# Performance work log

Measured on AMD Instinct MI355X. Metric: run time of the kernel, lower is better.

The kernel has to match this reference:

```python
import jax, jax.numpy as jnp
import numpy as np

NW, S, D, H, F = 4096, 64, 128, 8, 256
DH = D // H
EPS = 1e-5


def setup_inputs() -> dict:
    key = jax.random.key(0)
    ks = jax.random.split(key, 16)
    feat = jax.random.normal(ks[0], (NW, S, D), jnp.float32)
    pos = 0.1 * jax.random.normal(ks[1], (NW, S, D), jnp.float32)
    # each window has between S//2 and S valid voxels; True = padded key
    valid = jax.random.randint(ks[2], (NW, 1), S // 2, S + 1)
    mask = jnp.arange(S)[None, :] >= valid  # [NW, S] bool
    s = 1.0 / np.sqrt(D)
    u = lambda k, sh, sc: jax.random.uniform(k, sh, jnp.float32, -sc, sc)
    return {
        'feat': feat, 'pos': pos, 'mask': mask,
        'Wq': u(ks[3], (D, D), s), 'bq': jnp.zeros((D,), jnp.float32),
        'Wk': u(ks[4], (D, D), s), 'bk': jnp.zeros((D,), jnp.float32),
        'Wv': u(ks[5], (D, D), s), 'bv': jnp.zeros((D,), jnp.float32),
        'Wo': u(ks[6], (D, D), s), 'bo': jnp.zeros((D,), jnp.float32),
        'W1': u(ks[7], (D, F), s), 'b1': jnp.zeros((F,), jnp.float32),
        'W2': u(ks[8], (F, D), 1.0 / np.sqrt(F)), 'b2': jnp.zeros((D,), jnp.float32),
        'g1': jnp.ones((D,), jnp.float32), 'be1': jnp.zeros((D,), jnp.float32),
        'g2': jnp.ones((D,), jnp.float32), 'be2': jnp.zeros((D,), jnp.float32),
    }


def _layernorm(x, g, b):
    mu = jnp.mean(x, -1, keepdims=True)
    var = jnp.mean(jnp.square(x - mu), -1, keepdims=True)
    return (x - mu) * jax.lax.rsqrt(var + EPS) * g + b


def reference(feat, pos, mask, Wq, bq, Wk, bk, Wv, bv, Wo, bo,
              W1, b1, W2, b2, g1, be1, g2, be2):
    # windowed MHA: q = k = feat + pos, v = feat  (all windows batched)
    qk_in = feat + pos
    q = (qk_in @ Wq + bq).reshape(NW, S, H, DH)
    k = (qk_in @ Wk + bk).reshape(NW, S, H, DH)
    v = (feat @ Wv + bv).reshape(NW, S, H, DH)
    scores = jnp.einsum('wqhd,wkhd->whqk', q, k) / np.sqrt(DH)
    scores = jnp.where(mask[:, None, None, :], -1e9, scores)
    attn = jax.nn.softmax(scores, axis=-1)
    ctx = jnp.einsum('whqk,wkhd->wqhd', attn, v).reshape(NW, S, D)
    src2 = ctx @ Wo + bo
    # residual + LN + FFN + residual + LN (dropout = identity at eval)
    src = _layernorm(feat + src2, g1, be1)
    ffn = jax.nn.relu(src @ W1 + b1) @ W2 + b2
    return _layernorm(src + ffn, g2, be2)
```

## Files before the change

kernel.cpp:

```cpp
#include <hip/hip_runtime.h>

typedef __attribute__((ext_vector_type(8))) short bf16x8;
typedef __attribute__((ext_vector_type(4))) float f32x4;
typedef unsigned short u16;
typedef unsigned int u32;

#define MFMA16(a, b, c) __builtin_amdgcn_mfma_f32_16x16x32_bf16((a), (b), (c), 0, 0, 0)
#define CFENCE() asm volatile("" ::: "memory")


__device__ __forceinline__ u16 f2bf(float f) {
    union { float f; u32 u; } c; c.f = f;
    u32 r = c.u + 0x7fffu + ((c.u >> 16) & 1u);
    return (u16)(r >> 16);
}

__device__ __forceinline__ bf16x8 pack8(f32x4 a, f32x4 b) {
    union { u32 w[4]; bf16x8 v; } r;
    asm("v_cvt_pk_bf16_f32 %0, %1, %2" : "=v"(r.w[0]) : "v"(a[0]), "v"(a[1]));
    asm("v_cvt_pk_bf16_f32 %0, %1, %2" : "=v"(r.w[1]) : "v"(a[2]), "v"(a[3]));
    asm("v_cvt_pk_bf16_f32 %0, %1, %2" : "=v"(r.w[2]) : "v"(b[0]), "v"(b[1]));
    asm("v_cvt_pk_bf16_f32 %0, %1, %2" : "=v"(r.w[3]) : "v"(b[2]), "v"(b[3]));
    return r.v;
}

__device__ __forceinline__ void stage_h(const float* __restrict__ W, int ld,
                                        int n0, int k0, u16* __restrict__ sW,
                                        int t) {
#pragma unroll
    for (int i = 0; i < 4; ++i) {
        int e = i * 512 + t;
        int n = e & 63, kq = e >> 6;
        const float* src = W + (size_t)(k0 + kq * 4) * ld + n0 + n;
        float a = src[0], b = src[ld], c = src[2 * ld], d = src[3 * ld];
        u32 lo, hi;
        asm("v_cvt_pk_bf16_f32 %0, %1, %2" : "=v"(lo) : "v"(a), "v"(b));
        asm("v_cvt_pk_bf16_f32 %0, %1, %2" : "=v"(hi) : "v"(c), "v"(d));
        uint2 pk; pk.x = lo; pk.y = hi;
        *(uint2*)(sW + n * 136 + kq * 4) = pk;
    }
}

__device__ __forceinline__ void gemm_h(const bf16x8 aF[4], const u16* __restrict__ sW,
                                       int lr, int lk, f32x4 acc[4]) {
#pragma unroll
    for (int ks = 0; ks < 4; ++ks)
#pragma unroll
        for (int nt = 0; nt < 4; ++nt) {
            bf16x8 b = *(const bf16x8*)(sW + (nt * 16 + lr) * 136 + ks * 32 + lk * 8);
            acc[nt] = MFMA16(aF[ks], b, acc[nt]);
        }
}

__device__ __forceinline__ void row_ln(const f32x4 v[8], float mu[4], float rs[4]) {
#pragma unroll
    for (int r = 0; r < 4; ++r) {
        float s = 0.f;
#pragma unroll
        for (int nt = 0; nt < 8; ++nt) s += v[nt][r];
        s += __shfl_xor(s, 1); s += __shfl_xor(s, 2);
        s += __shfl_xor(s, 4); s += __shfl_xor(s, 8);
        float m_ = s * 0.0078125f;
        float q = 0.f;
#pragma unroll
        for (int nt = 0; nt < 8; ++nt) { float d = v[nt][r] - m_; q += d * d; }
        q += __shfl_xor(q, 1); q += __shfl_xor(q, 2);
        q += __shfl_xor(q, 4); q += __shfl_xor(q, 8);
        mu[r] = m_;
        rs[r] = rsqrtf(q * 0.0078125f + 1e-5f);
    }
}

__global__ __launch_bounds__(512) void enc_main(
    const float* __restrict__ feat, const float* __restrict__ pos,
    const unsigned char* __restrict__ maskb,
    const float* __restrict__ Wq, const float* __restrict__ bq,
    const float* __restrict__ Wk, const float* __restrict__ bk,
    const float* __restrict__ Wv, const float* __restrict__ bv,
    const float* __restrict__ Wo, const float* __restrict__ bo,
    const float* __restrict__ W1, const float* __restrict__ b1,
    const float* __restrict__ W2, const float* __restrict__ b2,
    const float* __restrict__ g1, const float* __restrict__ be1,
    const float* __restrict__ g2, const float* __restrict__ be2,
    float* __restrict__ out) {
    __shared__ __align__(16) char smem[142336];

    const int tid  = threadIdx.x;
    const int lane = tid & 63;
    const int wid  = tid >> 6;
    const int ww   = wid >> 2;
    const int m0   = (wid & 3) * 16;
    const int lr   = lane & 15;
    const int lk   = lane >> 4;
    const int w    = blockIdx.x * 2 + ww;

    char* wb   = smem + ww * 62464;
    u16* sQ    = (u16*)wb;
    u16* sK    = (u16*)(wb + 17408);
    u16* sVt   = (u16*)(wb + 34816);
    u16* sAttn = (u16*)(wb + 53248);
    u16* sF1   = (u16*)(wb + 17408);
    u16* sW    = (u16*)(smem + 124928);

    const float* fw = feat + (size_t)w * 8192;
    const float* pw = pos  + (size_t)w * 8192;

    stage_h(Wq, 128, 0, 0, sW, tid);

    int vld;
    {
        unsigned char smp = maskb[lane * 64 + 63];
        int ones = __popcll(__ballot(smp != 0));
        int m = (ones > 32) ? (maskb[(size_t)w * 64 + lane] != 0)
                            : (((const int*)maskb)[(size_t)w * 64 + lane] != 0);
        vld = 64 - __popcll(__ballot(m));
    }

    bf16x8 aX[4], aFv[4];
#pragma unroll
    for (int ks = 0; ks < 4; ++ks) {
        const float* fp = fw + (m0 + lr) * 128 + ks * 32 + lk * 8;
        const float* pp = pw + (m0 + lr) * 128 + ks * 32 + lk * 8;
        f32x4 f0 = *(const f32x4*)fp;
        f32x4 f1 = *(const f32x4*)(fp + 4);
        f32x4 p0 = *(const f32x4*)pp;
        f32x4 p1 = *(const f32x4*)(pp + 4);
        aFv[ks] = pack8(f0, f1);
        aX[ks]  = pack8(f0 + p0, f1 + p1);
    }
    __syncthreads();

#pragma unroll
    for (int hf = 0; hf < 2; ++hf) {
        f32x4 acc[4] = {};
        gemm_h(aX, sW, lr, lk, acc);
#pragma unroll
        for (int nt = 0; nt < 4; ++nt) {
            int col = hf * 64 + nt * 16 + lr; float bb = bq[col];
#pragma unroll
            for (int r = 0; r < 4; ++r)
                sQ[(m0 + lk * 4 + r) * 136 + col] = f2bf(acc[nt][r] + bb);
        }
        __syncthreads();
        if (hf == 0) stage_h(Wq, 128, 64, 0, sW, tid);
        else         stage_h(Wk, 128, 0, 0, sW, tid);
        __syncthreads();
    }
#pragma unroll
    for (int hf = 0; hf < 2; ++hf) {
        f32x4 acc[4] = {};
        gemm_h(aX, sW, lr, lk, acc);
#pragma unroll
        for (int nt = 0; nt < 4; ++nt) {
            int col = hf * 64 + nt * 16 + lr; float bb = bk[col];
#pragma unroll
            for (int r = 0; r < 4; ++r)
                sK[(m0 + lk * 4 + r) * 136 + col] = f2bf(acc[nt][r] + bb);
        }
        __syncthreads();
        if (hf == 0) stage_h(Wk, 128, 64, 0, sW, tid);
        else         stage_h(Wv, 128, 0, 0, sW, tid);
        __syncthreads();
    }
#pragma unroll
    for (int hf = 0; hf < 2; ++hf) {
        f32x4 acc[4] = {};
        gemm_h(aFv, sW, lr, lk, acc);
#pragma unroll
        for (int nt = 0; nt < 4; ++nt) {
            int dcol = hf * 64 + nt * 16 + lr; float bb = bv[dcol];
            float e0 = acc[nt][0] + bb, e1 = acc[nt][1] + bb;
            float e2 = acc[nt][2] + bb, e3 = acc[nt][3] + bb;
            u32 lo, hi;
            asm("v_cvt_pk_bf16_f32 %0, %1, %2" : "=v"(lo) : "v"(e0), "v"(e1));
            asm("v_cvt_pk_bf16_f32 %0, %1, %2" : "=v"(hi) : "v"(e2), "v"(e3));
            uint2 pk; pk.x = lo; pk.y = hi;
            *(uint2*)(sVt + dcol * 72 + m0 + lk * 4) = pk;
        }
        __syncthreads();
        if (hf == 0) { stage_h(Wv, 128, 64, 0, sW, tid); __syncthreads(); }
    }

    stage_h(Wo, 128, 0, 0, sW, tid);
    const int dup = (lk & 1) * 8;
#pragma unroll 1
    for (int h = 0; h < 8; ++h) {
        bf16x8 aQ = *(const bf16x8*)(sQ + (m0 + lr) * 136 + h * 16 + dup);
        f32x4 sc[4];
#pragma unroll
        for (int nt = 0; nt < 4; ++nt) {
            bf16x8 bK = *(const bf16x8*)(sK + (nt * 16 + lr) * 136 + h * 16 + dup);
            f32x4 zz = {0.f, 0.f, 0.f, 0.f};
            sc[nt] = MFMA16(aQ, bK, zz);
        }
#pragma unroll
        for (int nt = 0; nt < 4; ++nt) {
            bool msk = (nt * 16 + lr) >= vld;
#pragma unroll
            for (int r = 0; r < 4; ++r) {
                float v0 = sc[nt][r] * 0.125f;
                sc[nt][r] = msk ? -1e9f : v0;
            }
        }
        float mx[4], sm[4];
#pragma unroll
        for (int r = 0; r < 4; ++r) {
            float m_ = fmaxf(fmaxf(sc[0][r], sc[1][r]), fmaxf(sc[2][r], sc[3][r]));
            m_ = fmaxf(m_, __shfl_xor(m_, 1));
            m_ = fmaxf(m_, __shfl_xor(m_, 2));
            m_ = fmaxf(m_, __shfl_xor(m_, 4));
            m_ = fmaxf(m_, __shfl_xor(m_, 8));
            mx[r] = m_; sm[r] = 0.f;
        }
#pragma unroll
        for (int nt = 0; nt < 4; ++nt)
#pragma unroll
            for (int r = 0; r < 4; ++r) {
                float e = __expf(sc[nt][r] - mx[r]);
                sc[nt][r] = e; sm[r] += e;
            }
#pragma unroll
        for (int r = 0; r < 4; ++r) {
            float s_ = sm[r];
            s_ += __shfl_xor(s_, 1); s_ += __shfl_xor(s_, 2);
            s_ += __shfl_xor(s_, 4); s_ += __shfl_xor(s_, 8);
            sm[r] = 1.f / s_;
        }
#pragma unroll
        for (int nt = 0; nt < 4; ++nt)
#pragma unroll
            for (int r = 0; r < 4; ++r)
                sAttn[(m0 + lk * 4 + r) * 72 + nt * 16 + lr] = f2bf(sc[nt][r] * sm[r]);
        CFENCE();
        f32x4 cc = {0.f, 0.f, 0.f, 0.f};
#pragma unroll
        for (int ks = 0; ks < 2; ++ks) {
            bf16x8 aP = *(const bf16x8*)(sAttn + (m0 + lr) * 72 + ks * 32 + lk * 8);
            bf16x8 bV = *(const bf16x8*)(sVt + (h * 16 + lr) * 72 + ks * 32 + lk * 8);
            cc = MFMA16(aP, bV, cc);
        }
#pragma unroll
        for (int r = 0; r < 4; ++r)
            sQ[(m0 + lk * 4 + r) * 136 + h * 16 + lr] = f2bf(cc[r]);
    }
    CFENCE();
    __syncthreads();

    bf16x8 aC[4];
#pragma unroll
    for (int ks = 0; ks < 4; ++ks)
        aC[ks] = *(const bf16x8*)(sQ + (m0 + lr) * 136 + ks * 32 + lk * 8);
    f32x4 v8[8];
#pragma unroll
    for (int hf = 0; hf < 2; ++hf) {
        f32x4 acc[4] = {};
        gemm_h(aC, sW, lr, lk, acc);
#pragma unroll
        for (int nt = 0; nt < 4; ++nt) {
            int col = hf * 64 + nt * 16 + lr; float bb = bo[col];
#pragma unroll
            for (int r = 0; r < 4; ++r)
                v8[hf * 4 + nt][r] = acc[nt][r] + bb + fw[(m0 + lk * 4 + r) * 128 + col];
        }
        __syncthreads();
        if (hf == 0) stage_h(Wo, 128, 64, 0, sW, tid);
        else         stage_h(W1, 256, 0, 0, sW, tid);
        __syncthreads();
    }
    float mu[4], rs[4];
    row_ln(v8, mu, rs);
    f32x4 srcv[8];
#pragma unroll
    for (int nt = 0; nt < 8; ++nt) {
        int col = nt * 16 + lr;
        float gg = g1[col], bb = be1[col];
#pragma unroll
        for (int r = 0; r < 4; ++r) {
            float sv = (v8[nt][r] - mu[r]) * rs[r] * gg + bb;
            srcv[nt][r] = sv;
            sQ[(m0 + lk * 4 + r) * 136 + col] = f2bf(sv);
        }
    }
    CFENCE();
    bf16x8 aS[4];
#pragma unroll
    for (int ks = 0; ks < 4; ++ks)
        aS[ks] = *(const bf16x8*)(sQ + (m0 + lr) * 136 + ks * 32 + lk * 8);

#pragma unroll
    for (int hf = 0; hf < 4; ++hf) {
        f32x4 f1a[4] = {};
        gemm_h(aS, sW, lr, lk, f1a);
#pragma unroll
        for (int nt = 0; nt < 4; ++nt) {
            int col = hf * 64 + nt * 16 + lr; float bb = b1[col];
#pragma unroll
            for (int r = 0; r < 4; ++r)
                sF1[(m0 + lk * 4 + r) * 264 + col] = f2bf(fmaxf(f1a[nt][r] + bb, 0.f));
        }
        __syncthreads();
        if (hf < 3) stage_h(W1, 256, (hf + 1) * 64, 0, sW, tid);
        else        stage_h(W2, 128, 0, 0, sW, tid);
        __syncthreads();
    }

    f32x4 oa[8] = {};
#pragma unroll
    for (int s = 0; s < 4; ++s) {
        int kh = s >> 1, nh = s & 1;
#pragma unroll
        for (int ks = 0; ks < 4; ++ks) {
            bf16x8 aF = *(const bf16x8*)(sF1 + (m0 + lr) * 264 + kh * 128 + ks * 32 + lk * 8);
#pragma unroll
            for (int nt = 0; nt < 4; ++nt) {
                bf16x8 b = *(const bf16x8*)(sW + (nt * 16 + lr) * 136 + ks * 32 + lk * 8);
                oa[nh * 4 + nt] = MFMA16(aF, b, oa[nh * 4 + nt]);
            }
        }
        if (s < 3) {
            __syncthreads();
            int ns = s + 1, nkh = ns >> 1, nnh = ns & 1;
            stage_h(W2, 128, nnh * 64, nkh * 128, sW, tid);
            __syncthreads();
        }
    }

#pragma unroll
    for (int nt = 0; nt < 8; ++nt) {
        int col = nt * 16 + lr; float bb = b2[col];
#pragma unroll
        for (int r = 0; r < 4; ++r)
            v8[nt][r] = oa[nt][r] + bb + srcv[nt][r];
    }
    row_ln(v8, mu, rs);
    float* ow = out + (size_t)w * 8192;
#pragma unroll
    for (int nt = 0; nt < 8; ++nt) {
        int col = nt * 16 + lr;
        float gg = g2[col], bb = be2[col];
#pragma unroll
        for (int r = 0; r < 4; ++r)
            ow[(m0 + lk * 4 + r) * 128 + col] = (v8[nt][r] - mu[r]) * rs[r] * gg + bb;
    }
}

extern "C" void kernel_launch(void* const* d_in, const int* in_sizes, int n_in,
                              void* d_out, int out_size, void* d_ws, size_t ws_size,
                              hipStream_t stream) {
    (void)in_sizes; (void)n_in; (void)out_size; (void)d_ws; (void)ws_size;
    const float* feat = (const float*)d_in[0];
    const float* pos  = (const float*)d_in[1];
    const unsigned char* mask = (const unsigned char*)d_in[2];
    const float* Wq = (const float*)d_in[3];  const float* bq = (const float*)d_in[4];
    const float* Wk = (const float*)d_in[5];  const float* bk = (const float*)d_in[6];
    const float* Wv = (const float*)d_in[7];  const float* bv = (const float*)d_in[8];
    const float* Wo = (const float*)d_in[9];  const float* bo = (const float*)d_in[10];
    const float* W1 = (const float*)d_in[11]; const float* b1 = (const float*)d_in[12];
    const float* W2 = (const float*)d_in[13]; const float* b2 = (const float*)d_in[14];
    const float* g1 = (const float*)d_in[15]; const float* be1 = (const float*)d_in[16];
    const float* g2 = (const float*)d_in[17]; const float* be2 = (const float*)d_in[18];

    enc_main<<<2048, 512, 0, stream>>>(feat, pos, mask,
                                       Wq, bq, Wk, bk, Wv, bv, Wo, bo,
                                       W1, b1, W2, b2, g1, be1, g2, be2,
                                       (float*)d_out);
}
```

Baseline: 349.4 us.

## Double-buffer weight panels in shared memory to overlap staging with GEMMs

Replaces the single shared weight panel with two ping-pong panels, so the next weight half-panel is staged while the current one feeds the MFMA GEMMs. This removes one barrier per stage and lets the global weight loads overlap compute in the QKV, output projection and FFN phases. In exchange, LDS use per block grows to about 156 KB, which may limit occupancy, and correctness now depends on the alternating panel schedule being kept consistent.

```diff
diff --git a/kernel.cpp b/kernel.cpp
--- a/kernel.cpp
+++ b/kernel.cpp
@@ -83,7 +83,7 @@
     const float* __restrict__ g1, const float* __restrict__ be1,
     const float* __restrict__ g2, const float* __restrict__ be2,
     float* __restrict__ out) {
-    __shared__ __align__(16) char smem[142336];
+    __shared__ __align__(16) char smem[159744];
 
     const int tid  = threadIdx.x;
     const int lane = tid & 63;
@@ -100,12 +100,13 @@
     u16* sVt   = (u16*)(wb + 34816);
     u16* sAttn = (u16*)(wb + 53248);
     u16* sF1   = (u16*)(wb + 17408);
-    u16* sW    = (u16*)(smem + 124928);
+    u16* panA  = (u16*)(smem + 124928);
+    u16* panB  = (u16*)(smem + 142336);
 
     const float* fw = feat + (size_t)w * 8192;
     const float* pw = pos  + (size_t)w * 8192;
 
-    stage_h(Wq, 128, 0, 0, sW, tid);
+    stage_h(Wq, 128, 0, 0, panA, tid);
 
     int vld;
     {
@@ -130,45 +131,65 @@
     }
     __syncthreads();
 
-#pragma unroll
-    for (int hf = 0; hf < 2; ++hf) {
-        f32x4 acc[4] = {};
-        gemm_h(aX, sW, lr, lk, acc);
-#pragma unroll
-        for (int nt = 0; nt < 4; ++nt) {
-            int col = hf * 64 + nt * 16 + lr; float bb = bq[col];
+    {
+        stage_h(Wq, 128, 64, 0, panB, tid);
+        f32x4 acc[4] = {};
+        gemm_h(aX, panA, lr, lk, acc);
+#pragma unroll
+        for (int nt = 0; nt < 4; ++nt) {
+            int col = nt * 16 + lr; float bb = bq[col];
 #pragma unroll
             for (int r = 0; r < 4; ++r)
                 sQ[(m0 + lk * 4 + r) * 136 + col] = f2bf(acc[nt][r] + bb);
         }
         __syncthreads();
-        if (hf == 0) stage_h(Wq, 128, 64, 0, sW, tid);
-        else         stage_h(Wk, 128, 0, 0, sW, tid);
-        __syncthreads();
-    }
-#pragma unroll
-    for (int hf = 0; hf < 2; ++hf) {
-        f32x4 acc[4] = {};
-        gemm_h(aX, sW, lr, lk, acc);
-#pragma unroll
-        for (int nt = 0; nt < 4; ++nt) {
-            int col = hf * 64 + nt * 16 + lr; float bb = bk[col];
+    }
+    {
+        stage_h(Wk, 128, 0, 0, panA, tid);
+        f32x4 acc[4] = {};
+        gemm_h(aX, panB, lr, lk, acc);
+#pragma unroll
+        for (int nt = 0; nt < 4; ++nt) {
+            int col = 64 + nt * 16 + lr; float bb = bq[col];
+#pragma unroll
+            for (int r = 0; r < 4; ++r)
+                sQ[(m0 + lk * 4 + r) * 136 + col] = f2bf(acc[nt][r] + bb);
+        }
+        __syncthreads();
+    }
+    {
+        stage_h(Wk, 128, 64, 0, panB, tid);
+        f32x4 acc[4] = {};
+        gemm_h(aX, panA, lr, lk, acc);
+#pragma unroll
+        for (int nt = 0; nt < 4; ++nt) {
+            int col = nt * 16 + lr; float bb = bk[col];
 #pragma unroll
             for (int r = 0; r < 4; ++r)
                 sK[(m0 + lk * 4 + r) * 136 + col] = f2bf(acc[nt][r] + bb);
         }
         __syncthreads();
-        if (hf == 0) stage_h(Wk, 128, 64, 0, sW, tid);
-        else         stage_h(Wv, 128, 0, 0, sW, tid);
-        __syncthreads();
-    }
-#pragma unroll
-    for (int hf = 0; hf < 2; ++hf) {
-        f32x4 acc[4] = {};
-        gemm_h(aFv, sW, lr, lk, acc);
-#pragma unroll
-        for (int nt = 0; nt < 4; ++nt) {
-            int dcol = hf * 64 + nt * 16 + lr; float bb = bv[dcol];
+    }
+    {
+        stage_h(Wv, 128, 0, 0, panA, tid);
+        f32x4 acc[4] = {};
+        gemm_h(aX, panB, lr, lk, acc);
+#pragma unroll
+        for (int nt = 0; nt < 4; ++nt) {
+            int col = 64 + nt * 16 + lr; float bb = bk[col];
+#pragma unroll
+            for (int r = 0; r < 4; ++r)
+                sK[(m0 + lk * 4 + r) * 136 + col] = f2bf(acc[nt][r] + bb);
+        }
+        __syncthreads();
+    }
+    {
+        stage_h(Wv, 128, 64, 0, panB, tid);
+        f32x4 acc[4] = {};
+        gemm_h(aFv, panA, lr, lk, acc);
+#pragma unroll
+        for (int nt = 0; nt < 4; ++nt) {
+            int dcol = nt * 16 + lr; float bb = bv[dcol];
             float e0 = acc[nt][0] + bb, e1 = acc[nt][1] + bb;
             float e2 = acc[nt][2] + bb, e3 = acc[nt][3] + bb;
             u32 lo, hi;
@@ -178,10 +199,26 @@
             *(uint2*)(sVt + dcol * 72 + m0 + lk * 4) = pk;
         }
         __syncthreads();
-        if (hf == 0) { stage_h(Wv, 128, 64, 0, sW, tid); __syncthreads(); }
-    }
-
-    stage_h(Wo, 128, 0, 0, sW, tid);
+    }
+    {
+        stage_h(Wo, 128, 0, 0, panA, tid);
+        f32x4 acc[4] = {};
+        gemm_h(aFv, panB, lr, lk, acc);
+#pragma unroll
+        for (int nt = 0; nt < 4; ++nt) {
+            int dcol = 64 + nt * 16 + lr; float bb = bv[dcol];
+            float e0 = acc[nt][0] + bb, e1 = acc[nt][1] + bb;
+            float e2 = acc[nt][2] + bb, e3 = acc[nt][3] + bb;
+            u32 lo, hi;
+            asm("v_cvt_pk_bf16_f32 %0, %1, %2" : "=v"(lo) : "v"(e0), "v"(e1));
+            asm("v_cvt_pk_bf16_f32 %0, %1, %2" : "=v"(hi) : "v"(e2), "v"(e3));
+            uint2 pk; pk.x = lo; pk.y = hi;
+            *(uint2*)(sVt + dcol * 72 + m0 + lk * 4) = pk;
+        }
+        __syncthreads();
+    }
+
+    stage_h(Wo, 128, 64, 0, panB, tid);
     const int dup = (lk & 1) * 8;
 #pragma unroll 1
     for (int h = 0; h < 8; ++h) {
@@ -251,20 +288,29 @@
     for (int ks = 0; ks < 4; ++ks)
         aC[ks] = *(const bf16x8*)(sQ + (m0 + lr) * 136 + ks * 32 + lk * 8);
     f32x4 v8[8];
-#pragma unroll
-    for (int hf = 0; hf < 2; ++hf) {
-        f32x4 acc[4] = {};
-        gemm_h(aC, sW, lr, lk, acc);
-#pragma unroll
-        for (int nt = 0; nt < 4; ++nt) {
-            int col = hf * 64 + nt * 16 + lr; float bb = bo[col];
-#pragma unroll
-            for (int r = 0; r < 4; ++r)
-                v8[hf * 4 + nt][r] = acc[nt][r] + bb + fw[(m0 + lk * 4 + r) * 128 + col];
-        }
-        __syncthreads();
-        if (hf == 0) stage_h(Wo, 128, 64, 0, sW, tid);
-        else         stage_h(W1, 256, 0, 0, sW, tid);
+    {
+        f32x4 acc[4] = {};
+        gemm_h(aC, panA, lr, lk, acc);
+#pragma unroll
+        for (int nt = 0; nt < 4; ++nt) {
+            int col = nt * 16 + lr; float bb = bo[col];
+#pragma unroll
+            for (int r = 0; r < 4; ++r)
+                v8[nt][r] = acc[nt][r] + bb + fw[(m0 + lk * 4 + r) * 128 + col];
+        }
+        __syncthreads();
+    }
+    {
+        stage_h(W1, 256, 0, 0, panA, tid);
+        f32x4 acc[4] = {};
+        gemm_h(aC, panB, lr, lk, acc);
+#pragma unroll
+        for (int nt = 0; nt < 4; ++nt) {
+            int col = 64 + nt * 16 + lr; float bb = bo[col];
+#pragma unroll
+            for (int r = 0; r < 4; ++r)
+                v8[4 + nt][r] = acc[nt][r] + bb + fw[(m0 + lk * 4 + r) * 128 + col];
+        }
         __syncthreads();
     }
     float mu[4], rs[4];
@@ -289,8 +335,12 @@
 
 #pragma unroll
     for (int hf = 0; hf < 4; ++hf) {
+        u16* cur = (hf & 1) ? panB : panA;
+        u16* nxt = (hf & 1) ? panA : panB;
+        if (hf < 3) stage_h(W1, 256, (hf + 1) * 64, 0, nxt, tid);
+        else        stage_h(W2, 128, 0, 0, nxt, tid);
         f32x4 f1a[4] = {};
-        gemm_h(aS, sW, lr, lk, f1a);
+        gemm_h(aS, cur, lr, lk, f1a);
 #pragma unroll
         for (int nt = 0; nt < 4; ++nt) {
             int col = hf * 64 + nt * 16 + lr; float bb = b1[col];
@@ -299,30 +349,28 @@
                 sF1[(m0 + lk * 4 + r) * 264 + col] = f2bf(fmaxf(f1a[nt][r] + bb, 0.f));
         }
         __syncthreads();
-        if (hf < 3) stage_h(W1, 256, (hf + 1) * 64, 0, sW, tid);
-        else        stage_h(W2, 128, 0, 0, sW, tid);
-        __syncthreads();
     }
 
     f32x4 oa[8] = {};
 #pragma unroll
     for (int s = 0; s < 4; ++s) {
+        u16* cur = (s & 1) ? panB : panA;
+        u16* nxt = (s & 1) ? panA : panB;
+        if (s < 3) {
+            int ns = s + 1, nkh = ns >> 1, nnh = ns & 1;
+            stage_h(W2, 128, nnh * 64, nkh * 128, nxt, tid);
+        }
         int kh = s >> 1, nh = s & 1;
 #pragma unroll
         for (int ks = 0; ks < 4; ++ks) {
             bf16x8 aF = *(const bf16x8*)(sF1 + (m0 + lr) * 264 + kh * 128 + ks * 32 + lk * 8);
 #pragma unroll
             for (int nt = 0; nt < 4; ++nt) {
-                bf16x8 b = *(const bf16x8*)(sW + (nt * 16 + lr) * 136 + ks * 32 + lk * 8);
+                bf16x8 b = *(const bf16x8*)(cur + (nt * 16 + lr) * 136 + ks * 32 + lk * 8);
                 oa[nh * 4 + nt] = MFMA16(aF, b, oa[nh * 4 + nt]);
             }
         }
-        if (s < 3) {
-            __syncthreads();
-            int ns = s + 1, nkh = ns >> 1, nnh = ns & 1;
-            stage_h(W2, 128, nnh * 64, nkh * 128, sW, tid);
-            __syncthreads();
-        }
+        if (s < 3) __syncthreads();
     }
 
 #pragma unroll
```

Result: faster. 334.3 us (median of 2 runs) (-4.3%).
